# Optimization experiments

Measured on AMD Instinct MI355X. Metric: run time of the kernel, lower is better.

## Reference

```python
import jax, jax.numpy as jnp
import numpy as np

S, B, D, H = 4096, 4, 1024, 16
DH = D // H


def _xavier(key, fan_in, fan_out):
    bound = float(np.sqrt(6.0 / (fan_in + fan_out)))
    return jax.random.uniform(key, (fan_out, fan_in), jnp.float32, -bound, bound)


def setup_inputs() -> dict:
    key = jax.random.key(0)
    kq, kk, kv, kwq, kwk, kwv = jax.random.split(key, 6)
    return {
        "q": jax.random.normal(kq, (S, B, D), jnp.float32),
        "k": jax.random.normal(kk, (S, B, D), jnp.float32),
        "v": jax.random.normal(kv, (S, B, D), jnp.float32),
        "Wq": _xavier(kwq, D, D),
        "Wk": _xavier(kwk, D, D),
        "Wv": _xavier(kwv, D, D),
    }


def reference(q, k, v, Wq, Wk, Wv):
    s, b = q.shape[:2]
    # exp feature maps after bias-free linear projections (nn.Linear: x @ W.T)
    q_h = jnp.exp(q @ Wq.T).reshape(s, b, H, DH)
    k_h = jnp.exp(k @ Wk.T).reshape(s, b, H, DH)
    v_h = (v @ Wv.T).reshape(s, b, H, DH)
    # original: einsum('sbnd,sbnde->sbne', q, k[...,None]*v[None...]) / same-with-ones
    # contract over d without materializing the (s,b,n,d,e) outer product
    qk = jnp.einsum('sbnd,sbnd->sbn', q_h, k_h)[..., None]  # (s,b,n,1)
    out = (qk * v_h) / qk                                   # (s,b,n,dh)
    out = out.reshape(s, b, D)
    return jnp.cumsum(out, axis=1)  # cumsum over dim=1 (batch), as in source
```

## Files before the change

### kernel.cpp

```cpp
#include <hip/hip_runtime.h>
#include <hip/hip_bf16.h>


typedef short s16x8 __attribute__((ext_vector_type(8)));
typedef float f32x4 __attribute__((ext_vector_type(4)));

constexpr int M_ = 16384, N_ = 1024, K_ = 1024;
constexpr int BM = 256, BN = 128, BK = 32;
constexpr int KS = 32;
constexpr size_t WS_NEED = 2097152;

static __device__ __forceinline__ unsigned cvtpk(float lo, float hi) {
  unsigned r;
  asm("v_cvt_pk_bf16_f32 %0, %1, %2" : "=v"(r) : "v"(lo), "v"(hi));
  return r;
}

__global__ __launch_bounds__(256) void cvt_w(const float* __restrict__ w,
                                             unsigned short* __restrict__ wb) {
  const int t0 = blockIdx.x * 256 + threadIdx.x;
#pragma unroll
  for (int r = 0; r < 4; ++r) {
    const int i = t0 + r * 65536;
    float4 x = ((const float4*)w)[i];
    uint2 p; p.x = cvtpk(x.x, x.y); p.y = cvtpk(x.z, x.w);
    ((uint2*)wb)[i] = p;
  }
}

__global__ __launch_bounds__(512, 4) void la_gemm9(
    const float* __restrict__ Vp,
    const unsigned short* __restrict__ Bb,
    float* __restrict__ out) {
  __shared__ __align__(16) char lds[2][24576];
  char* ldsb = (char*)lds;

  const int tid = threadIdx.x, lane = tid & 63, wave = tid >> 6;
  const int wr = wave >> 1, wc = wave & 1;
  const int l15 = lane & 15;

  const int gid = blockIdx.x;
  const int xcd = gid & 7, t = gid >> 3;
  const int mt = xcd * 8 + (t >> 3);
  const int nt = t & 7;

  const int ar = tid >> 1, ah = tid & 1;
  const float* sAp = Vp + (size_t)(mt * 256 + ar) * K_ + ah * 16;
  const int as = (ar >> 1) & 3;
  const int wbA0 = ar * 64 + (((2 * ah)     ^ as) << 4);
  const int wbA1 = ar * 64 + (((2 * ah + 1) ^ as) << 4);

  const int cg = ((lane & 3) ^ ((lane >> 3) & 3)) << 4;
  const char* srcB = (const char*)Bb +
      (size_t)(nt * 128 + wave * 16 + (lane >> 2)) * 2048 + cg;
  const int ldsB = 16384 + wave * 1024;

  const int lswz = (((lane >> 4) ^ ((l15 >> 1) & 3)) << 4);
  const int rdA = (wr * 64 + l15) * 64 + lswz;
  const int rdB = 16384 + (wc * 64 + l15) * 64 + lswz;

  f32x4 acc[4][4] = {};
  float4 sa0, sa1, sa2, sa3;

#define LOADA(kt) do {                                                        \
    const float* p_ = sAp + (kt) * BK;                                        \
    sa0 = *(const float4*)p_;      sa1 = *(const float4*)(p_ + 4);            \
    sa2 = *(const float4*)(p_ + 8); sa3 = *(const float4*)(p_ + 12);          \
  } while (0)

#define GLLB(kt, buf)                                                         \
  __builtin_amdgcn_global_load_lds(                                           \
      (__attribute__((address_space(1))) void*)(void*)(srcB + (kt) * 64),     \
      (__attribute__((address_space(3))) void*)(void*)(ldsb + (buf) * 24576 + ldsB), \
      16, 0, 0)

#define WRITEA(buf) do {                                                      \
    char* A_ = ldsb + (buf) * 24576;                                          \
    uint4 w0_, w1_;                                                           \
    w0_.x = cvtpk(sa0.x, sa0.y); w0_.y = cvtpk(sa0.z, sa0.w);                 \
    w0_.z = cvtpk(sa1.x, sa1.y); w0_.w = cvtpk(sa1.z, sa1.w);                 \
    w1_.x = cvtpk(sa2.x, sa2.y); w1_.y = cvtpk(sa2.z, sa2.w);                 \
    w1_.z = cvtpk(sa3.x, sa3.y); w1_.w = cvtpk(sa3.z, sa3.w);                 \
    *(uint4*)(A_ + wbA0) = w0_;                                               \
    *(uint4*)(A_ + wbA1) = w1_;                                               \
  } while (0)

#define COMPUTE(buf) do {                                                     \
    const char* U_ = ldsb + (buf) * 24576;                                    \
    s16x8 af[4], bf[4];                                                       \
    _Pragma("unroll") for (int n_ = 0; n_ < 4; ++n_)                          \
      bf[n_] = *(const s16x8*)(U_ + rdB + n_ * 1024);                         \
    _Pragma("unroll") for (int m_ = 0; m_ < 4; ++m_)                          \
      af[m_] = *(const s16x8*)(U_ + rdA + m_ * 1024);                         \
    __builtin_amdgcn_s_setprio(1);                                            \
    _Pragma("unroll") for (int m_ = 0; m_ < 4; ++m_)                          \
    _Pragma("unroll") for (int n_ = 0; n_ < 4; ++n_)                          \
        acc[m_][n_] = __builtin_amdgcn_mfma_f32_16x16x32_bf16(                \
            af[m_], bf[n_], acc[m_][n_], 0, 0, 0);                            \
    __builtin_amdgcn_s_setprio(0);                                            \
  } while (0)

  GLLB(0, 0);
  LOADA(0);
  WRITEA(0);
  __syncthreads();

  for (int kt = 0; kt < KS; ++kt) {
    const int cur = kt & 1;
    const bool pf = (kt + 1 < KS);
    if (pf) { GLLB(kt + 1, cur ^ 1); LOADA(kt + 1); }
    COMPUTE(cur);
    if (pf) WRITEA(cur ^ 1);
    __syncthreads();
  }

#pragma unroll
  for (int m = 0; m < 4; ++m) {
    const int row0 = mt * 256 + wr * 64 + m * 16 + ((lane >> 4) << 2);
#pragma unroll
    for (int n = 0; n < 4; ++n) {
      f32x4 a = acc[m][n];
      a.y += a.x;  a.z += a.y;  a.w += a.z;
      const int col = nt * 128 + wc * 64 + n * 16 + l15;
      out[(size_t)(row0 + 0) * N_ + col] = a.x;
      out[(size_t)(row0 + 1) * N_ + col] = a.y;
      out[(size_t)(row0 + 2) * N_ + col] = a.z;
      out[(size_t)(row0 + 3) * N_ + col] = a.w;
    }
  }
#undef LOADA
#undef GLLB
#undef WRITEA
#undef COMPUTE
}

__global__ __launch_bounds__(512, 2) void la_gemm_fb(
    const float* __restrict__ Vp, const float* __restrict__ Wp, float* __restrict__ out) {
  extern __shared__ char lds[];
  const int tid = threadIdx.x, lane = tid & 63, wave = tid >> 6;
  const int wr = wave >> 2, wc = wave & 3;
  const int gid = blockIdx.x, xcd = gid & 7, q = gid >> 3;
  const int mt = xcd * 8 + (q >> 2), nt = q & 3;
  const int srow = tid >> 3, schunk = tid & 7;
  const float* sAp = Vp + (size_t)(mt * 256 + srow) * K_ + schunk * 8;
  const float* sBp = Wp + (size_t)(nt * 256 + srow) * K_ + schunk * 8;
  const int wbyte = srow * 128 + ((schunk ^ (srow & 7)) << 4);
  const int basa0 = (wr * 128 + (lane & 15)) * 128 + (((lane >> 4) ^ (lane & 7)) << 4);
  const int basb0 = (wc * 64 + (lane & 15)) * 128 + (((lane >> 4) ^ (lane & 7)) << 4);
  f32x4 acc[8][4] = {};
  float4 sa[8], sb[8];
  auto loadset = [&](int kt) {
#pragma unroll
    for (int i = 0; i < 4; ++i) {
      const float* pa = sAp + kt * 64 + i * (64 * K_);
      const float* pb = sBp + kt * 64 + i * (64 * K_);
      sa[2*i] = *(const float4*)pa; sa[2*i+1] = *(const float4*)(pa + 4);
      sb[2*i] = *(const float4*)pb; sb[2*i+1] = *(const float4*)(pb + 4);
    }
  };
  auto cvtwrite = [&](int buf) {
    char* A = lds + buf * 65536; char* B = A + 32768;
#pragma unroll
    for (int i = 0; i < 4; ++i) {
      uint4 wa, wb;
      wa.x = cvtpk(sa[2*i].x, sa[2*i].y);     wa.y = cvtpk(sa[2*i].z, sa[2*i].w);
      wa.z = cvtpk(sa[2*i+1].x, sa[2*i+1].y); wa.w = cvtpk(sa[2*i+1].z, sa[2*i+1].w);
      wb.x = cvtpk(sb[2*i].x, sb[2*i].y);     wb.y = cvtpk(sb[2*i].z, sb[2*i].w);
      wb.z = cvtpk(sb[2*i+1].x, sb[2*i+1].y); wb.w = cvtpk(sb[2*i+1].z, sb[2*i+1].w);
      *(uint4*)(A + wbyte + i * 8192) = wa;
      *(uint4*)(B + wbyte + i * 8192) = wb;
    }
  };
  auto compute = [&](int buf) {
    const char* A = lds + buf * 65536; const char* B = A + 32768;
#pragma unroll
    for (int kk = 0; kk < 2; ++kk) {
      const int ba = basa0 ^ (kk ? 64 : 0), bb = basb0 ^ (kk ? 64 : 0);
      s16x8 bf[4];
#pragma unroll
      for (int n = 0; n < 4; ++n) bf[n] = *(const s16x8*)(B + bb + n * 2048);
#pragma unroll
      for (int mh = 0; mh < 2; ++mh) {
        s16x8 af[4];
#pragma unroll
        for (int m = 0; m < 4; ++m) af[m] = *(const s16x8*)(A + ba + (mh * 4 + m) * 2048);
        __builtin_amdgcn_s_setprio(1);
#pragma unroll
        for (int m = 0; m < 4; ++m)
#pragma unroll
          for (int n = 0; n < 4; ++n)
            acc[mh*4+m][n] = __builtin_amdgcn_mfma_f32_16x16x32_bf16(af[m], bf[n], acc[mh*4+m][n], 0, 0, 0);
        __builtin_amdgcn_s_setprio(0);
      }
    }
  };
  loadset(0); cvtwrite(0); __syncthreads();
  for (int kt = 0; kt < 16; ++kt) {
    const int cur = kt & 1;
    if (kt + 1 < 16) loadset(kt + 1);
    compute(cur);
    if (kt + 1 < 16) cvtwrite(cur ^ 1);
    __syncthreads();
  }
#pragma unroll
  for (int m = 0; m < 8; ++m) {
    const int row0 = mt * 256 + wr * 128 + m * 16 + ((lane >> 4) << 2);
#pragma unroll
    for (int n = 0; n < 4; ++n) {
      f32x4 a = acc[m][n];
      a.y += a.x; a.z += a.y; a.w += a.z;
      const int col = nt * 256 + wc * 64 + n * 16 + (lane & 15);
      out[(size_t)(row0 + 0) * N_ + col] = a.x;
      out[(size_t)(row0 + 1) * N_ + col] = a.y;
      out[(size_t)(row0 + 2) * N_ + col] = a.z;
      out[(size_t)(row0 + 3) * N_ + col] = a.w;
    }
  }
}

extern "C" void kernel_launch(void* const* d_in, const int* in_sizes, int n_in,
                              void* d_out, int out_size, void* d_ws, size_t ws_size,
                              hipStream_t stream) {
  const float* v  = (const float*)d_in[2];
  const float* Wv = (const float*)d_in[5];
  float* out = (float*)d_out;
  (void)in_sizes; (void)n_in; (void)out_size;

  if (ws_size >= WS_NEED) {
    unsigned short* wb = (unsigned short*)d_ws;
    cvt_w<<<dim3(256), dim3(256), 0, stream>>>(Wv, wb);
    la_gemm9<<<dim3(512), dim3(512), 0, stream>>>(v, wb, out);
  } else {
    hipFuncSetAttribute((const void*)la_gemm_fb,
                        hipFuncAttributeMaxDynamicSharedMemorySize, 131072);
    la_gemm_fb<<<dim3(256), dim3(512), 131072, stream>>>(v, Wv, out);
  }
}
```

Before: 59.52 us.

## Enlarge GEMM tile to 256x256 with BK=64 and split compute around A conversion

Replaces the 256x128, BK=32 tile kernel with a 256x256 tile, BK=64 kernel using 128KB of dynamic LDS and 256 blocks. Each wave now holds an 8x4 MFMA accumulator grid, which doubles arithmetic intensity and halves the A re-reads from global memory. The A bf16 convert-and-write is placed between the two k-halves of compute so it overlaps with MFMA work. The cost is fewer blocks (256 on the device), lower occupancy and higher register pressure.

```diff
diff --git a/kernel.cpp b/kernel.cpp
--- a/kernel.cpp
+++ b/kernel.cpp
@@ -6,8 +6,7 @@
 typedef float f32x4 __attribute__((ext_vector_type(4)));
 
 constexpr int M_ = 16384, N_ = 1024, K_ = 1024;
-constexpr int BM = 256, BN = 128, BK = 32;
-constexpr int KS = 32;
+constexpr int KT = 16;
 constexpr size_t WS_NEED = 2097152;
 
 static __device__ __forceinline__ unsigned cvtpk(float lo, float hi) {
@@ -28,76 +27,99 @@
   }
 }
 
-__global__ __launch_bounds__(512, 4) void la_gemm9(
+#define GLL(srcp, ldsoff)                                                     \
+  __builtin_amdgcn_global_load_lds(                                           \
+      (__attribute__((address_space(1))) void*)(void*)(srcp),                 \
+      (__attribute__((address_space(3))) void*)(void*)(lds + (ldsoff)),       \
+      16, 0, 0)
+
+__global__ __launch_bounds__(512, 2) void la_gemm11(
     const float* __restrict__ Vp,
     const unsigned short* __restrict__ Bb,
     float* __restrict__ out) {
-  __shared__ __align__(16) char lds[2][24576];
-  char* ldsb = (char*)lds;
+  extern __shared__ char lds[];
 
   const int tid = threadIdx.x, lane = tid & 63, wave = tid >> 6;
-  const int wr = wave >> 1, wc = wave & 1;
-  const int l15 = lane & 15;
+  const int wr = wave >> 2, wc = wave & 3;
+  const int l15 = lane & 15, l7 = lane & 7, l3 = lane >> 3;
 
   const int gid = blockIdx.x;
-  const int xcd = gid & 7, t = gid >> 3;
-  const int mt = xcd * 8 + (t >> 3);
-  const int nt = t & 7;
-
-  const int ar = tid >> 1, ah = tid & 1;
-  const float* sAp = Vp + (size_t)(mt * 256 + ar) * K_ + ah * 16;
-  const int as = (ar >> 1) & 3;
-  const int wbA0 = ar * 64 + (((2 * ah)     ^ as) << 4);
-  const int wbA1 = ar * 64 + (((2 * ah + 1) ^ as) << 4);
-
-  const int cg = ((lane & 3) ^ ((lane >> 3) & 3)) << 4;
-  const char* srcB = (const char*)Bb +
-      (size_t)(nt * 128 + wave * 16 + (lane >> 2)) * 2048 + cg;
-  const int ldsB = 16384 + wave * 1024;
-
-  const int lswz = (((lane >> 4) ^ ((l15 >> 1) & 3)) << 4);
-  const int rdA = (wr * 64 + l15) * 64 + lswz;
-  const int rdB = 16384 + (wc * 64 + l15) * 64 + lswz;
-
-  f32x4 acc[4][4] = {};
-  float4 sa0, sa1, sa2, sa3;
+  const int xcd = gid & 7, q = gid >> 3;
+  const int mt = xcd * 8 + (q >> 2), nt = q & 3;
+
+  const int srow = tid >> 3, schunk = tid & 7;
+  const float* sAp = Vp + (size_t)(mt * 256 + srow) * K_ + schunk * 8;
+  const int wbyte = srow * 128 + ((schunk ^ (srow & 7)) << 4);
+
+  const int sch = ((l7 ^ l3) & 7) << 4;
+  const char* sB[2][2];
+#pragma unroll
+  for (int h = 0; h < 2; ++h)
+#pragma unroll
+    for (int j = 0; j < 2; ++j)
+      sB[h][j] = (const char*)Bb +
+          (size_t)(nt * 256 + h * 128 + j * 64 + wave * 8 + l3) * 2048 + sch;
+  const int ldsBw = wave * 1024;
+
+  const int basa = wr * 16384 + l15 * 128 + (((lane >> 4) ^ l7) << 4);
+  const int basb = (wc * 64 + l15) * 128 + (((lane >> 4) ^ l7) << 4);
+
+  f32x4 acc[8][4] = {};
+  float4 sa[8];
 
 #define LOADA(kt) do {                                                        \
-    const float* p_ = sAp + (kt) * BK;                                        \
-    sa0 = *(const float4*)p_;      sa1 = *(const float4*)(p_ + 4);            \
-    sa2 = *(const float4*)(p_ + 8); sa3 = *(const float4*)(p_ + 12);          \
-  } while (0)
-
-#define GLLB(kt, buf)                                                         \
-  __builtin_amdgcn_global_load_lds(                                           \
-      (__attribute__((address_space(1))) void*)(void*)(srcB + (kt) * 64),     \
-      (__attribute__((address_space(3))) void*)(void*)(ldsb + (buf) * 24576 + ldsB), \
-      16, 0, 0)
+    _Pragma("unroll")                                                         \
+    for (int i_ = 0; i_ < 4; ++i_) {                                          \
+      const float* p_ = sAp + (kt) * 64 + i_ * (64 * K_);                     \
+      sa[2*i_]   = *(const float4*)p_;                                        \
+      sa[2*i_+1] = *(const float4*)(p_ + 4);                                  \
+    }                                                                         \
+  } while (0)
 
 #define WRITEA(buf) do {                                                      \
-    char* A_ = ldsb + (buf) * 24576;                                          \
-    uint4 w0_, w1_;                                                           \
-    w0_.x = cvtpk(sa0.x, sa0.y); w0_.y = cvtpk(sa0.z, sa0.w);                 \
-    w0_.z = cvtpk(sa1.x, sa1.y); w0_.w = cvtpk(sa1.z, sa1.w);                 \
-    w1_.x = cvtpk(sa2.x, sa2.y); w1_.y = cvtpk(sa2.z, sa2.w);                 \
-    w1_.z = cvtpk(sa3.x, sa3.y); w1_.w = cvtpk(sa3.z, sa3.w);                 \
-    *(uint4*)(A_ + wbA0) = w0_;                                               \
-    *(uint4*)(A_ + wbA1) = w1_;                                               \
-  } while (0)
-
-#define COMPUTE(buf) do {                                                     \
-    const char* U_ = ldsb + (buf) * 24576;                                    \
-    s16x8 af[4], bf[4];                                                       \
-    _Pragma("unroll") for (int n_ = 0; n_ < 4; ++n_)                          \
-      bf[n_] = *(const s16x8*)(U_ + rdB + n_ * 1024);                         \
-    _Pragma("unroll") for (int m_ = 0; m_ < 4; ++m_)                          \
-      af[m_] = *(const s16x8*)(U_ + rdA + m_ * 1024);                         \
-    __builtin_amdgcn_s_setprio(1);                                            \
-    _Pragma("unroll") for (int m_ = 0; m_ < 4; ++m_)                          \
-    _Pragma("unroll") for (int n_ = 0; n_ < 4; ++n_)                          \
-        acc[m_][n_] = __builtin_amdgcn_mfma_f32_16x16x32_bf16(                \
-            af[m_], bf[n_], acc[m_][n_], 0, 0, 0);                            \
-    __builtin_amdgcn_s_setprio(0);                                            \
+    char* A_ = lds + (buf) * 32768;                                           \
+    _Pragma("unroll")                                                         \
+    for (int i_ = 0; i_ < 4; ++i_) {                                          \
+      uint4 w_;                                                               \
+      w_.x = cvtpk(sa[2*i_].x,   sa[2*i_].y);                                 \
+      w_.y = cvtpk(sa[2*i_].z,   sa[2*i_].w);                                 \
+      w_.z = cvtpk(sa[2*i_+1].x, sa[2*i_+1].y);                               \
+      w_.w = cvtpk(sa[2*i_+1].z, sa[2*i_+1].w);                               \
+      *(uint4*)(A_ + wbyte + i_ * 8192) = w_;                                 \
+    }                                                                         \
+  } while (0)
+
+#define GLLB(kt, buf) do {                                                    \
+    const int bb_ = 65536 + (buf) * 32768;                                    \
+    GLL(sB[0][0] + (kt) * 128, bb_ + 0     + ldsBw);                          \
+    GLL(sB[0][1] + (kt) * 128, bb_ + 8192  + ldsBw);                          \
+    GLL(sB[1][0] + (kt) * 128, bb_ + 16384 + ldsBw);                          \
+    GLL(sB[1][1] + (kt) * 128, bb_ + 24576 + ldsBw);                          \
+  } while (0)
+
+#define COMPUTE_KK(buf, kk) do {                                              \
+    const char* A_ = lds + (buf) * 32768;                                     \
+    const char* B_ = lds + 65536 + (buf) * 32768;                             \
+    const int xo_ = (kk) ? 64 : 0;                                            \
+    s16x8 bf[4];                                                              \
+    _Pragma("unroll")                                                         \
+    for (int n_ = 0; n_ < 4; ++n_)                                            \
+      bf[n_] = *(const s16x8*)(B_ + ((basb + n_ * 2048) ^ xo_));              \
+    _Pragma("unroll")                                                         \
+    for (int mh_ = 0; mh_ < 2; ++mh_) {                                       \
+      s16x8 af[4];                                                            \
+      _Pragma("unroll")                                                       \
+      for (int m_ = 0; m_ < 4; ++m_)                                          \
+        af[m_] = *(const s16x8*)(A_ + ((basa + (mh_*4 + m_) * 2048) ^ xo_));  \
+      __builtin_amdgcn_s_setprio(1);                                          \
+      _Pragma("unroll")                                                       \
+      for (int m_ = 0; m_ < 4; ++m_)                                          \
+        _Pragma("unroll")                                                     \
+        for (int n_ = 0; n_ < 4; ++n_)                                        \
+          acc[mh_*4 + m_][n_] = __builtin_amdgcn_mfma_f32_16x16x32_bf16(      \
+              af[m_], bf[n_], acc[mh_*4 + m_][n_], 0, 0, 0);                  \
+      __builtin_amdgcn_s_setprio(0);                                         \
+    }                                                                         \
   } while (0)
 
   GLLB(0, 0);
@@ -105,23 +127,24 @@
   WRITEA(0);
   __syncthreads();
 
-  for (int kt = 0; kt < KS; ++kt) {
+  for (int kt = 0; kt < KT; ++kt) {
     const int cur = kt & 1;
-    const bool pf = (kt + 1 < KS);
+    const bool pf = (kt + 1 < KT);
     if (pf) { GLLB(kt + 1, cur ^ 1); LOADA(kt + 1); }
-    COMPUTE(cur);
+    COMPUTE_KK(cur, 0);
     if (pf) WRITEA(cur ^ 1);
+    COMPUTE_KK(cur, 1);
     __syncthreads();
   }
 
 #pragma unroll
-  for (int m = 0; m < 4; ++m) {
-    const int row0 = mt * 256 + wr * 64 + m * 16 + ((lane >> 4) << 2);
+  for (int m = 0; m < 8; ++m) {
+    const int row0 = mt * 256 + wr * 128 + m * 16 + ((lane >> 4) << 2);
 #pragma unroll
     for (int n = 0; n < 4; ++n) {
       f32x4 a = acc[m][n];
       a.y += a.x;  a.z += a.y;  a.w += a.z;
-      const int col = nt * 128 + wc * 64 + n * 16 + l15;
+      const int col = nt * 256 + wc * 64 + n * 16 + l15;
       out[(size_t)(row0 + 0) * N_ + col] = a.x;
       out[(size_t)(row0 + 1) * N_ + col] = a.y;
       out[(size_t)(row0 + 2) * N_ + col] = a.z;
@@ -129,9 +152,9 @@
     }
   }
 #undef LOADA
+#undef WRITEA
 #undef GLLB
-#undef WRITEA
-#undef COMPUTE
+#undef COMPUTE_KK
 }
 
 __global__ __launch_bounds__(512, 2) void la_gemm_fb(
@@ -149,6 +172,9 @@
   const int basb0 = (wc * 64 + (lane & 15)) * 128 + (((lane >> 4) ^ (lane & 7)) << 4);
   f32x4 acc[8][4] = {};
   float4 sa[8], sb[8];
+  auto cvtpk_ = [](float lo, float hi) {
+    unsigned r; asm("v_cvt_pk_bf16_f32 %0, %1, %2" : "=v"(r) : "v"(lo), "v"(hi)); return r;
+  };
   auto loadset = [&](int kt) {
 #pragma unroll
     for (int i = 0; i < 4; ++i) {
@@ -163,10 +189,10 @@
 #pragma unroll
     for (int i = 0; i < 4; ++i) {
       uint4 wa, wb;
-      wa.x = cvtpk(sa[2*i].x, sa[2*i].y);     wa.y = cvtpk(sa[2*i].z, sa[2*i].w);
-      wa.z = cvtpk(sa[2*i+1].x, sa[2*i+1].y); wa.w = cvtpk(sa[2*i+1].z, sa[2*i+1].w);
-      wb.x = cvtpk(sb[2*i].x, sb[2*i].y);     wb.y = cvtpk(sb[2*i].z, sb[2*i].w);
-      wb.z = cvtpk(sb[2*i+1].x, sb[2*i+1].y); wb.w = cvtpk(sb[2*i+1].z, sb[2*i+1].w);
+      wa.x = cvtpk_(sa[2*i].x, sa[2*i].y);     wa.y = cvtpk_(sa[2*i].z, sa[2*i].w);
+      wa.z = cvtpk_(sa[2*i+1].x, sa[2*i+1].y); wa.w = cvtpk_(sa[2*i+1].z, sa[2*i+1].w);
+      wb.x = cvtpk_(sb[2*i].x, sb[2*i].y);     wb.y = cvtpk_(sb[2*i].z, sb[2*i].w);
+      wb.z = cvtpk_(sb[2*i+1].x, sb[2*i+1].y); wb.w = cvtpk_(sb[2*i+1].z, sb[2*i+1].w);
       *(uint4*)(A + wbyte + i * 8192) = wa;
       *(uint4*)(B + wbyte + i * 8192) = wb;
     }
@@ -229,7 +255,9 @@
   if (ws_size >= WS_NEED) {
     unsigned short* wb = (unsigned short*)d_ws;
     cvt_w<<<dim3(256), dim3(256), 0, stream>>>(Wv, wb);
-    la_gemm9<<<dim3(512), dim3(512), 0, stream>>>(v, wb, out);
+    hipFuncSetAttribute((const void*)la_gemm11,
+                        hipFuncAttributeMaxDynamicSharedMemorySize, 131072);
+    la_gemm11<<<dim3(256), dim3(512), 131072, stream>>>(v, wb, out);
   } else {
     hipFuncSetAttribute((const void*)la_gemm_fb,
                         hipFuncAttributeMaxDynamicSharedMemorySize, 131072);
```

Result: faster. 51.87 us (-12.9%).
